# Kernel tuning notes

Measured on AMD Instinct MI355X. Metric: run time of the kernel, lower is better.

Reference implementation:

```python
import jax, jax.numpy as jnp
import numpy as np
from jax import lax

B, S, I = 256, 16, 64
D = 128
N_ITEMS = 100000
K = 3
PAD_ID = 0
BOS_ID = N_ITEMS
DILATIONS = (1, 2, 4)


def setup_inputs() -> dict:
    key = jax.random.key(0)
    ks = jax.random.split(key, 16)
    item_id = jax.random.randint(ks[0], (B, S, I), 0, N_ITEMS, dtype=jnp.int32)
    eval_from = jax.random.randint(ks[1], (B,), 0, S, dtype=jnp.int32)
    u_type = jax.random.randint(ks[2], (B,), 0, 4, dtype=jnp.int32)
    emb = jax.random.normal(ks[3], (N_ITEMS + 1, D), jnp.float32) * 0.05
    emb = emb.at[PAD_ID].set(0.0)  # padding_idx=0
    kaiming = (2.0 / (D * K)) ** 0.5
    conv_w0 = jax.random.normal(ks[4], (D, D, K), jnp.float32) * kaiming
    conv_w1 = jax.random.normal(ks[5], (D, D, K), jnp.float32) * kaiming
    conv_w2 = jax.random.normal(ks[6], (D, D, K), jnp.float32) * kaiming
    conv_b0 = jnp.zeros((D,), jnp.float32)
    conv_b1 = jnp.zeros((D,), jnp.float32)
    conv_b2 = jnp.zeros((D,), jnp.float32)
    gru_wih = jax.random.normal(ks[7], (3 * D, D), jnp.float32) * 0.05
    gru_whh = jax.random.normal(ks[8], (3 * D, D), jnp.float32) * 0.05
    gru_bih = jax.random.normal(ks[9], (3 * D,), jnp.float32) * 0.05
    gru_bhh = jax.random.normal(ks[10], (3 * D,), jnp.float32) * 0.05
    fus_w = jax.random.normal(ks[11], (D, 2 * D), jnp.float32) * 0.05
    fus_b = jnp.zeros((D,), jnp.float32)
    return {"item_id": item_id, "eval_from": eval_from, "u_type": u_type,
            "emb": emb,
            "conv_w0": conv_w0, "conv_b0": conv_b0,
            "conv_w1": conv_w1, "conv_b1": conv_b1,
            "conv_w2": conv_w2, "conv_b2": conv_b2,
            "gru_wih": gru_wih, "gru_whh": gru_whh,
            "gru_bih": gru_bih, "gru_bhh": gru_bhh,
            "fus_w": fus_w, "fus_b": fus_b}


def reference(item_id, eval_from, u_type, emb,
              conv_w0, conv_b0, conv_w1, conv_b1, conv_w2, conv_b2,
              gru_wih, gru_whh, gru_bih, gru_bhh, fus_w, fus_b):
    item_id = jnp.maximum(item_id, 0)  # clamp_min(0)
    Bc, Sc, Ic = item_id.shape
    convs = ((conv_w0, conv_b0, DILATIONS[0]),
             (conv_w1, conv_b1, DILATIONS[1]),
             (conv_w2, conv_b2, DILATIONS[2]))

    def tcn(x):  # x: [B, T, D] -> [B, T, D]
        h = jnp.transpose(x, (0, 2, 1))  # NCH
        for w, b, dil in convs:
            pad = (K - 1) * dil
            out = lax.conv_general_dilated(
                h, w, window_strides=(1,), padding=[(pad, 0)],
                rhs_dilation=(dil,),
                dimension_numbers=('NCH', 'OIH', 'NCH')) + b[None, :, None]
            h = jax.nn.relu(out + h)
        return jnp.transpose(h, (0, 2, 1))

    def gru_step(h, x):  # h,x: [B, D]
        gi = x @ gru_wih.T + gru_bih
        gh = h @ gru_whh.T + gru_bhh
        ir, iz, inn = jnp.split(gi, 3, axis=-1)
        hr, hz, hn = jnp.split(gh, 3, axis=-1)
        r = jax.nn.sigmoid(ir + hr)
        z = jax.nn.sigmoid(iz + hz)
        n = jnp.tanh(inn + r * hn)
        return (1.0 - z) * n + z * h

    pos = jnp.arange(Ic + 1)
    bos = jnp.full((Bc, 1), BOS_ID, dtype=item_id.dtype)

    def step(h, seq_s):  # seq_s: [B, I]
        lengths = (seq_s != PAD_ID).sum(-1)          # [B]
        max_len = lengths.max()                       # batch-level session max
        seq = jnp.concatenate([bos, seq_s], axis=1)   # [B, I+1], BOS prepended
        valid = pos[None, :] <= max_len               # positions torch keeps
        seq = jnp.where(valid, seq, PAD_ID)
        mask = seq != PAD_ID
        e = emb[seq]                                  # [B, I+1, D] (PAD row is 0)
        tc = tcn(e)
        fin = jnp.concatenate([tc, jnp.broadcast_to(h[:, None, :], tc.shape)], -1)
        reps = fin @ fus_w.T + fus_b                  # [B, I+1, D]
        reps = reps * valid[..., None]                # torch zero-pads beyond max_len
        # drop mask at last valid token (per-sample python loop in torch)
        mask = mask & ~((pos[None, :] == lengths[:, None]) & (lengths > 0)[:, None])
        mf = mask.astype(e.dtype)
        mean_emb = (e * mf[..., None]).sum(1) / jnp.maximum(mf.sum(1), 1.0)[:, None]
        h2 = gru_step(h, mean_emb)
        return h2, (reps, mask)

    h0 = jnp.zeros((Bc, D), jnp.float32)
    _, (reps, masks) = lax.scan(step, h0, jnp.transpose(item_id, (1, 0, 2)))
    reps = jnp.transpose(reps, (1, 0, 2, 3))          # [B, S, I+1, D]
    masks = jnp.transpose(masks, (1, 0, 2))           # [B, S, I+1]
    allow = jnp.arange(Sc)[None, :] >= eval_from[:, None]
    loss_masks = masks & allow[:, :, None]
    return reps, loss_masks, u_type
```

## Files before the change

kernel.cpp:

```cpp
#include <hip/hip_runtime.h>

#define BB 256
#define SS 16
#define II 64
#define DD 128
#define TT 65
#define BOS_ID 100000
#define RB 88
#define XBYTES (RB*256)

#define OFF_LEN  0
#define OFF_ML   16384
#define OFF_ME   32768
#define OFF_HB   (32768 + 2097152)
#define OFF_WB   (OFF_HB + 2097152)
#define OFF_FT   (OFF_WB + 294912)
#define OFF_WIHP (OFF_FT + 32768)
#define OFF_WGRU (OFF_WIHP + 98304)
#define OFF_GI   (OFF_WGRU + 131072)

#define OUT_MASK  (BB*SS*TT*DD)
#define OUT_UTYPE (OUT_MASK + BB*SS*TT)

typedef __attribute__((ext_vector_type(8))) short short8;
typedef __attribute__((ext_vector_type(4))) float f32x4;

__device__ __forceinline__ unsigned short f2bf(float f) {
    unsigned int u = __builtin_bit_cast(unsigned int, f);
    return (unsigned short)((u + 0x7fffu + ((u >> 16) & 1u)) >> 16);
}
__device__ __forceinline__ float bf2f(unsigned short h) {
    unsigned int u = ((unsigned int)h) << 16;
    return __builtin_bit_cast(float, u);
}
__device__ __forceinline__ void gld16(const void* g, void* l) {
    __builtin_amdgcn_global_load_lds(
        (const __attribute__((address_space(1))) void*)g,
        (__attribute__((address_space(3))) void*)l, 16, 0, 0);
}

__global__ __launch_bounds__(256) void prep_kernel(
    const float* __restrict__ w0, const float* __restrict__ w1,
    const float* __restrict__ w2, const float* __restrict__ fus_w,
    const float* __restrict__ wih, const float* __restrict__ whh,
    unsigned short* __restrict__ wB, unsigned short* __restrict__ fT,
    unsigned int* __restrict__ wihP, unsigned int* __restrict__ wgruP)
{
    int idx = blockIdx.x * 256 + threadIdx.x;
    if (idx < 147456) {
        int L  = idx / 49152;
        int r  = idx % 49152;
        int k  = r >> 14;
        int co = (r >> 7) & 127;
        int ci = r & 127;
        const float* w = (L == 0) ? w0 : ((L == 1) ? w1 : w2);
        float v = w[(co * 128 + ci) * 3 + k];
        wB[((L * 3 + k) * 128 + co) * 128 + (ci ^ ((co & 7) << 3))] = f2bf(v);
    } else if (idx < 163840) {
        int f  = idx - 147456;
        int j  = f >> 7;
        int ci = f & 127;
        fT[(j << 7) | (ci ^ ((j & 7) << 3))] = f2bf(fus_w[j * 256 + ci]);
    } else if (idx < 163840 + 24576) {
        int f  = idx - 163840;
        int dd = f / 384;
        int r  = f % 384;
        unsigned int lo = f2bf(wih[r * 128 + 2 * dd]);
        unsigned int hi = f2bf(wih[r * 128 + 2 * dd + 1]);
        wihP[f] = (hi << 16) | lo;
    } else if (idx < 163840 + 24576 + 32768) {
        int f  = idx - 163840 - 24576;
        int dd = f >> 9;
        int r  = f & 511;
        float v0, v1;
        if (r < 384) { v0 = whh[r * 128 + 2 * dd]; v1 = whh[r * 128 + 2 * dd + 1]; }
        else { const float* fw = fus_w + (r - 384) * 256 + 128;
               v0 = fw[2 * dd]; v1 = fw[2 * dd + 1]; }
        wgruP[f] = ((unsigned int)f2bf(v1) << 16) | (unsigned int)f2bf(v0);
    }
}

__global__ __launch_bounds__(256) void len_kernel(
    const int* __restrict__ item_id, const int* __restrict__ u_type,
    int* __restrict__ lengths, int* __restrict__ maxlen,
    float* __restrict__ u_out)
{
    int s = blockIdx.x;
    int b = threadIdx.x;
    const int* row = item_id + (b * SS + s) * II;
    int cnt = 0;
    for (int i = 0; i < II; ++i) cnt += (row[i] > 0);
    lengths[b * SS + s] = cnt;
    __shared__ int red[256];
    red[b] = cnt;
    __syncthreads();
    for (int off = 128; off > 0; off >>= 1) {
        if (b < off) red[b] = max(red[b], red[b + off]);
        __syncthreads();
    }
    if (b == 0) maxlen[s] = red[0];
    if (s == 0) u_out[b] = (float)u_type[b];
}

__global__ __launch_bounds__(128) void mean_kernel(
    const int* __restrict__ item_id, const int* __restrict__ eval_from,
    const float* __restrict__ emb,
    const int* __restrict__ lengths, const int* __restrict__ maxlen,
    float* __restrict__ mean_emb, float* __restrict__ mask_out)
{
    int bid = blockIdx.x;
    int b = bid >> 4, s = bid & 15;
    int tid = threadIdx.x;
    __shared__ int seqs[TT];
    __shared__ int msk[TT];
    int ml  = maxlen[s];
    int len = lengths[bid];
    int ef  = eval_from[b];
    if (tid < TT) {
        int v;
        if (tid == 0) v = BOS_ID;
        else { int it = item_id[bid * II + tid - 1]; v = it > 0 ? it : 0; }
        if (tid > ml) v = 0;
        int m = (v != 0) && !(tid == len && len > 0);
        seqs[tid] = v;
        msk[tid]  = m;
        mask_out[bid * TT + tid] = (m && (s >= ef)) ? 1.0f : 0.0f;
    }
    __syncthreads();
    int cnt = 0;
    for (int p = 0; p < TT; ++p) cnt += msk[p];
    float acc = 0.0f;
    int d = tid;
    for (int p = 0; p < TT; ++p) {
        if (msk[p]) acc += emb[seqs[p] * DD + d];
    }
    mean_emb[bid * DD + d] = acc / (float)max(cnt, 1);
}

__global__ __launch_bounds__(384, 1) void gi_kernel(
    const float* __restrict__ me_all, const unsigned int* __restrict__ wihP,
    const float* __restrict__ bih, float* __restrict__ gi_all)
{
    __shared__ __align__(16) unsigned int wl[64 * 384];
    __shared__ __align__(16) float me[DD];
    int t   = threadIdx.x;
    int blk = blockIdx.x;
    {
        const unsigned char* g = (const unsigned char*)wihP + t * 16;
        unsigned char* l = (unsigned char*)wl + t * 16;
#pragma unroll
        for (int i = 0; i < 16; ++i) gld16(g + i * 6144, l + i * 6144);
    }
    float bi = bih[t];
    asm volatile("s_waitcnt vmcnt(0)" ::: "memory");
    __syncthreads();
    for (int q = 0; q < 16; ++q) {
        int bs = blk * 16 + q;
        if (t < DD) me[t] = me_all[bs * DD + t];
        __syncthreads();
        float acc = bi;
#pragma unroll
        for (int dd = 0; dd < 64; ++dd) {
            unsigned int u = wl[dd * 384 + t];
            float f0 = __builtin_bit_cast(float, u << 16);
            float f1 = __builtin_bit_cast(float, u & 0xffff0000u);
            acc += f0 * me[2 * dd] + f1 * me[2 * dd + 1];
        }
        gi_all[bs * 384 + t] = acc;
        __syncthreads();
    }
}

__global__ __launch_bounds__(512, 1) void gru_kernel(
    const unsigned int* __restrict__ wgruP, const float* __restrict__ bhh,
    const float* __restrict__ fus_b, const float* __restrict__ gi_all,
    float* __restrict__ hB)
{
    __shared__ __align__(16) unsigned int wl[64 * 512];
    __shared__ float h[DD];
    __shared__ float g_z[DD], g_inn[DD], g_hn[DD];
    int t = threadIdx.x;
    int b = blockIdx.x;
    int j = t & 127;
    int grp = t >> 7;
    {
        const unsigned char* g = (const unsigned char*)wgruP + t * 16;
        unsigned char* l = (unsigned char*)wl + t * 16;
#pragma unroll
        for (int i = 0; i < 16; ++i) gld16(g + i * 8192, l + i * 8192);
    }
    float bias = (t < 384) ? bhh[t] : fus_b[j];
    if (t < DD) h[t] = 0.0f;
    asm volatile("s_waitcnt vmcnt(0)" ::: "memory");
    __syncthreads();
    for (int s = 0; s < SS; ++s) {
        float gi = (grp < 3) ? gi_all[(b * SS + s) * 384 + t] : 0.0f;
        float acc = bias;
#pragma unroll
        for (int dd = 0; dd < 64; ++dd) {
            unsigned int u = wl[dd * 512 + t];
            float f0 = __builtin_bit_cast(float, u << 16);
            float f1 = __builtin_bit_cast(float, u & 0xffff0000u);
            acc += f0 * h[2 * dd] + f1 * h[2 * dd + 1];
        }
        if (grp == 3) {
            hB[(s * BB + b) * DD + j] = acc;
        } else if (grp == 1) { g_z[j] = gi + acc; }
        else if (grp == 2)   { g_inn[j] = gi; g_hn[j] = acc; }
        __syncthreads();
        if (grp == 0) {
            float r = 1.0f / (1.0f + expf(-(gi + acc)));
            float z = 1.0f / (1.0f + expf(-g_z[j]));
            float n = tanhf(g_inn[j] + r * g_hn[j]);
            h[j] = (1.0f - z) * n + z * h[j];
        }
        __syncthreads();
    }
}

__global__ __launch_bounds__(256) void tcn_kernel(
    const int* __restrict__ item_id, const float* __restrict__ emb,
    const int* __restrict__ maxlen,
    const unsigned short* __restrict__ wB,
    const float* __restrict__ cb0, const float* __restrict__ cb1,
    const float* __restrict__ cb2,
    const unsigned short* __restrict__ fT, const float* __restrict__ hB,
    float* __restrict__ reps)
{
    __shared__ __align__(16) unsigned char xbufA[XBYTES];
    __shared__ __align__(16) unsigned char xbufB[XBYTES];
    __shared__ __align__(16) unsigned char wl[32768];
    __shared__ int seqs[TT];

    int tid  = threadIdx.x;
    int bid  = blockIdx.x;
    int b    = bid >> 4, s = bid & 15;
    int lane = tid & 63, wv = tid >> 6;
    int ml   = maxlen[s];

    if (tid < TT) {
        int v;
        if (tid == 0) v = BOS_ID;
        else { int it = item_id[bid * II + tid - 1]; v = it > 0 ? it : 0; }
        if (tid > ml) v = 0;
        seqs[tid] = v;
    }
    if (tid < 128) { *(unsigned int*)(xbufA + tid * 16) = 0u;
                     *(unsigned int*)(xbufA + tid * 16 + 4) = 0u;
                     *(unsigned int*)(xbufA + tid * 16 + 8) = 0u;
                     *(unsigned int*)(xbufA + tid * 16 + 12) = 0u; }
    else { int t = tid - 128;
           *(unsigned int*)(xbufB + t * 16) = 0u;
           *(unsigned int*)(xbufB + t * 16 + 4) = 0u;
           *(unsigned int*)(xbufB + t * 16 + 8) = 0u;
           *(unsigned int*)(xbufB + t * 16 + 12) = 0u; }
    __syncthreads();

    for (int p = wv; p < TT; p += 4) {
        const float* er = emb + (long)seqs[p] * DD + lane * 2;
        float f0 = er[0], f1 = er[1];
        int row = 8 + p;
        unsigned int pk = ((unsigned int)f2bf(f1) << 16) | (unsigned int)f2bf(f0);
        *(unsigned int*)(xbufA + row * 256 + ((lane * 4) ^ ((row & 7) << 4))) = pk;
    }

    unsigned char* xsrc = xbufA;
    unsigned char* ydst = xbufB;
    int co0  = wv * 32;
    int colb = (lane >> 4) * 16;

    f32x4 acc[5][2];

    for (int L = 0; L < 3; ++L) {
        int dil = 1 << L;
        const float* cb = (L == 0) ? cb0 : ((L == 1) ? cb1 : cb2);
#pragma unroll
        for (int mt = 0; mt < 5; ++mt)
#pragma unroll
            for (int nt = 0; nt < 2; ++nt)
#pragma unroll
                for (int r = 0; r < 4; ++r) acc[mt][nt][r] = 0.0f;

        for (int k = 0; k < 3; ++k) {
            __syncthreads();
            {
                const unsigned char* g =
                    (const unsigned char*)wB + (size_t)(L * 3 + k) * 32768 +
                    (wv * 64 + lane) * 16;
#pragma unroll
                for (int i = 0; i < 8; ++i)
                    gld16(g + i * 4096, wl + wv * 1024 + i * 4096);
            }
            asm volatile("s_waitcnt vmcnt(0)" ::: "memory");
            __syncthreads();

            int off = (2 - k) * dil;
#pragma unroll
            for (int cib = 0; cib < 4; ++cib) {
                int cbyte = cib * 64 + colb;
                short8 bfr[2];
#pragma unroll
                for (int nt = 0; nt < 2; ++nt) {
                    int rowB = co0 + nt * 16 + (lane & 15);
                    bfr[nt] = *(const short8*)(wl + rowB * 256 +
                                               (cbyte ^ ((rowB & 7) << 4)));
                }
#pragma unroll
                for (int mt = 0; mt < 5; ++mt) {
                    int rowA = 8 + mt * 16 + (lane & 15) - off;
                    short8 af = *(const short8*)(xsrc + rowA * 256 +
                                                 (cbyte ^ ((rowA & 7) << 4)));
                    acc[mt][0] = __builtin_amdgcn_mfma_f32_16x16x32_bf16(
                        af, bfr[0], acc[mt][0], 0, 0, 0);
                    acc[mt][1] = __builtin_amdgcn_mfma_f32_16x16x32_bf16(
                        af, bfr[1], acc[mt][1], 0, 0, 0);
                }
            }
        }
        float bias0 = cb[co0 + (lane & 15)];
        float bias1 = cb[co0 + 16 + (lane & 15)];
#pragma unroll
        for (int mt = 0; mt < 5; ++mt)
#pragma unroll
            for (int nt = 0; nt < 2; ++nt) {
                int co = co0 + nt * 16 + (lane & 15);
                float bia = nt ? bias1 : bias0;
#pragma unroll
                for (int r = 0; r < 4; ++r) {
                    int p = mt * 16 + (lane >> 4) * 4 + r;
                    if (p < TT) {
                        int row = 8 + p;
                        int xb2 = row * 256 + ((co * 2) ^ ((row & 7) << 4));
                        float v = acc[mt][nt][r] + bia +
                                  bf2f(*(const unsigned short*)(xsrc + xb2));
                        *(unsigned short*)(ydst + xb2) = f2bf(v > 0.f ? v : 0.f);
                    }
                }
            }
        unsigned char* t = xsrc; xsrc = ydst; ydst = t;
    }

    __syncthreads();
    {
        const unsigned char* g = (const unsigned char*)fT + (wv * 64 + lane) * 16;
#pragma unroll
        for (int i = 0; i < 8; ++i)
            gld16(g + i * 4096, wl + wv * 1024 + i * 4096);
    }
    asm volatile("s_waitcnt vmcnt(0)" ::: "memory");
    __syncthreads();

#pragma unroll
    for (int mt = 0; mt < 5; ++mt)
#pragma unroll
        for (int nt = 0; nt < 2; ++nt)
#pragma unroll
            for (int r = 0; r < 4; ++r) acc[mt][nt][r] = 0.0f;

#pragma unroll
    for (int cib = 0; cib < 4; ++cib) {
        int cbyte = cib * 64 + colb;
        short8 bfr[2];
#pragma unroll
        for (int nt = 0; nt < 2; ++nt) {
            int rowB = co0 + nt * 16 + (lane & 15);
            bfr[nt] = *(const short8*)(wl + rowB * 256 + (cbyte ^ ((rowB & 7) << 4)));
        }
#pragma unroll
        for (int mt = 0; mt < 5; ++mt) {
            int rowA = 8 + mt * 16 + (lane & 15);
            short8 af = *(const short8*)(xsrc + rowA * 256 +
                                         (cbyte ^ ((rowA & 7) << 4)));
            acc[mt][0] = __builtin_amdgcn_mfma_f32_16x16x32_bf16(
                af, bfr[0], acc[mt][0], 0, 0, 0);
            acc[mt][1] = __builtin_amdgcn_mfma_f32_16x16x32_bf16(
                af, bfr[1], acc[mt][1], 0, 0, 0);
        }
    }

    float hb0 = hB[(s * BB + b) * DD + co0 + (lane & 15)];
    float hb1 = hB[(s * BB + b) * DD + co0 + 16 + (lane & 15)];
    long obase = (long)bid * (TT * DD);
#pragma unroll
    for (int mt = 0; mt < 5; ++mt)
#pragma unroll
        for (int nt = 0; nt < 2; ++nt) {
            int j = co0 + nt * 16 + (lane & 15);
            float hb = nt ? hb1 : hb0;
#pragma unroll
            for (int r = 0; r < 4; ++r) {
                int p = mt * 16 + (lane >> 4) * 4 + r;
                if (p < TT) {
                    float v = (p <= ml) ? (acc[mt][nt][r] + hb) : 0.0f;
                    reps[obase + p * DD + j] = v;
                }
            }
        }
}

extern "C" void kernel_launch(void* const* d_in, const int* in_sizes, int n_in,
                              void* d_out, int out_size, void* d_ws, size_t ws_size,
                              hipStream_t stream) {
    const int*   item_id   = (const int*)  d_in[0];
    const int*   eval_from = (const int*)  d_in[1];
    const int*   u_type    = (const int*)  d_in[2];
    const float* emb       = (const float*)d_in[3];
    const float* conv_w0   = (const float*)d_in[4];
    const float* conv_b0   = (const float*)d_in[5];
    const float* conv_w1   = (const float*)d_in[6];
    const float* conv_b1   = (const float*)d_in[7];
    const float* conv_w2   = (const float*)d_in[8];
    const float* conv_b2   = (const float*)d_in[9];
    const float* gru_wih   = (const float*)d_in[10];
    const float* gru_whh   = (const float*)d_in[11];
    const float* gru_bih   = (const float*)d_in[12];
    const float* gru_bhh   = (const float*)d_in[13];
    const float* fus_w     = (const float*)d_in[14];
    const float* fus_b     = (const float*)d_in[15];

    char* ws = (char*)d_ws;
    int*            lengths  = (int*)           (ws + OFF_LEN);
    int*            maxlen   = (int*)           (ws + OFF_ML);
    float*          mean_emb = (float*)         (ws + OFF_ME);
    float*          hB       = (float*)         (ws + OFF_HB);
    unsigned short* wB       = (unsigned short*)(ws + OFF_WB);
    unsigned short* fT       = (unsigned short*)(ws + OFF_FT);
    unsigned int*   wihP     = (unsigned int*)  (ws + OFF_WIHP);
    unsigned int*   wgruP    = (unsigned int*)  (ws + OFF_WGRU);
    float*          gi_all   = (float*)         (ws + OFF_GI);

    float* out  = (float*)d_out;
    float* reps = out;
    float* mout = out + OUT_MASK;
    float* uout = out + OUT_UTYPE;

    prep_kernel<<<864, 256, 0, stream>>>(conv_w0, conv_w1, conv_w2, fus_w,
                                         gru_wih, gru_whh, wB, fT, wihP, wgruP);
    len_kernel<<<SS, 256, 0, stream>>>(item_id, u_type, lengths, maxlen, uout);
    mean_kernel<<<BB * SS, 128, 0, stream>>>(item_id, eval_from, emb, lengths, maxlen,
                                             mean_emb, mout);
    gi_kernel<<<BB, 384, 0, stream>>>(mean_emb, wihP, gru_bih, gi_all);
    gru_kernel<<<BB, 512, 0, stream>>>(wgruP, gru_bhh, fus_b, gi_all, hB);
    tcn_kernel<<<BB * SS, 256, 0, stream>>>(item_id, emb, maxlen, wB,
                                            conv_b0, conv_b1, conv_b2, fT, hB, reps);
}
```

Measured before the change: 292.6 us.

## Restructure TCN kernel: two tiles per block, per-wave double-buffered weight streaming

Each block of the TCN kernel now handles two (b,s) tiles, with a pair of waves per tile and each wave owning 64 output channels. Weights are pre-packed into per-wave 8 KB chunks covering conv layers and the fusion matrix, and streamed through a per-wave double-buffered LDS ring with async global-to-LDS loads. This removes most block-wide barriers and overlaps weight loads with MFMA work. Activations are updated in place in padded rows instead of an XOR swizzle with ping-pong buffers, and launch bounds request 2 blocks per CU. In exchange, each thread holds more accumulator registers and the LDS padding scheme must avoid bank conflicts.

```diff
diff --git a/kernel.cpp b/kernel.cpp
--- a/kernel.cpp
+++ b/kernel.cpp
@@ -6,16 +6,16 @@
 #define DD 128
 #define TT 65
 #define BOS_ID 100000
-#define RB 88
-#define XBYTES (RB*256)
+#define XROW 304
+#define XROWS 73
+#define XT (XROWS*XROW)
 
 #define OFF_LEN  0
 #define OFF_ML   16384
 #define OFF_ME   32768
 #define OFF_HB   (32768 + 2097152)
-#define OFF_WB   (OFF_HB + 2097152)
-#define OFF_FT   (OFF_WB + 294912)
-#define OFF_WIHP (OFF_FT + 32768)
+#define OFF_WB2  (OFF_HB + 2097152)
+#define OFF_WIHP (OFF_WB2 + 327680)
 #define OFF_WGRU (OFF_WIHP + 98304)
 #define OFF_GI   (OFF_WGRU + 131072)
 
@@ -43,24 +43,32 @@
     const float* __restrict__ w0, const float* __restrict__ w1,
     const float* __restrict__ w2, const float* __restrict__ fus_w,
     const float* __restrict__ wih, const float* __restrict__ whh,
-    unsigned short* __restrict__ wB, unsigned short* __restrict__ fT,
+    unsigned short* __restrict__ wB2,
     unsigned int* __restrict__ wihP, unsigned int* __restrict__ wgruP)
 {
     int idx = blockIdx.x * 256 + threadIdx.x;
-    if (idx < 147456) {
-        int L  = idx / 49152;
-        int r  = idx % 49152;
-        int k  = r >> 14;
-        int co = (r >> 7) & 127;
-        int ci = r & 127;
-        const float* w = (L == 0) ? w0 : ((L == 1) ? w1 : w2);
-        float v = w[(co * 128 + ci) * 3 + k];
-        wB[((L * 3 + k) * 128 + co) * 128 + (ci ^ ((co & 7) << 3))] = f2bf(v);
-    } else if (idx < 163840) {
-        int f  = idx - 147456;
-        int j  = f >> 7;
-        int ci = f & 127;
-        fT[(j << 7) | (ci ^ ((j & 7) << 3))] = f2bf(fus_w[j * 256 + ci]);
+    if (idx < 163840) {
+        int cid2  = idx >> 11;
+        int inner = idx & 2047;
+        int g = inner >> 9;
+        int c = (inner >> 3) & 63;
+        int e = inner & 7;
+        int nh   = cid2 & 1;
+        int rest = cid2 >> 1;
+        int cq   = rest & 3;
+        int m    = rest >> 2;
+        int ci = cq * 32 + g * 8 + e;
+        float v;
+        if (m < 9) {
+            int L = m / 3, k = m % 3;
+            int co = nh * 64 + c;
+            const float* w = (L == 0) ? w0 : ((L == 1) ? w1 : w2);
+            v = w[(co * 128 + ci) * 3 + k];
+        } else {
+            int j = nh * 64 + c;
+            v = fus_w[j * 256 + ci];
+        }
+        wB2[idx] = f2bf(v);
     } else if (idx < 163840 + 24576) {
         int f  = idx - 163840;
         int dd = f / 384;
@@ -218,181 +226,142 @@
     }
 }
 
-__global__ __launch_bounds__(256) void tcn_kernel(
+__global__ __launch_bounds__(256, 2) void tcn_kernel(
     const int* __restrict__ item_id, const float* __restrict__ emb,
     const int* __restrict__ maxlen,
-    const unsigned short* __restrict__ wB,
+    const unsigned short* __restrict__ wB2,
     const float* __restrict__ cb0, const float* __restrict__ cb1,
     const float* __restrict__ cb2,
-    const unsigned short* __restrict__ fT, const float* __restrict__ hB,
-    float* __restrict__ reps)
-{
-    __shared__ __align__(16) unsigned char xbufA[XBYTES];
-    __shared__ __align__(16) unsigned char xbufB[XBYTES];
-    __shared__ __align__(16) unsigned char wl[32768];
-    __shared__ int seqs[TT];
-
-    int tid  = threadIdx.x;
-    int bid  = blockIdx.x;
-    int b    = bid >> 4, s = bid & 15;
-    int lane = tid & 63, wv = tid >> 6;
-    int ml   = maxlen[s];
-
-    if (tid < TT) {
+    const float* __restrict__ hB, float* __restrict__ reps)
+{
+    __shared__ __align__(16) unsigned char lds_x[2][XT];
+    __shared__ __align__(16) unsigned char ring[4][2][4096];
+    __shared__ int seqs2[2][TT];
+
+    const int tid = threadIdx.x, bid = blockIdx.x;
+    const int lane = tid & 63, wv = tid >> 6;
+    const int l15 = lane & 15, q4 = lane >> 4;
+    const int t = wv >> 1, nh = wv & 1;
+    const int tile = bid * 2 + t;
+    const int b = tile >> 4, s = tile & 15;
+    const int ml = maxlen[s];
+
+    const unsigned char* wsrc = (const unsigned char*)wB2 + nh * 4096 + lane * 16;
+    unsigned char* xb = lds_x[t];
+
+    {
+#pragma unroll
+        for (int i = 0; i < 4; ++i) gld16(wsrc + i * 1024, &ring[wv][0][i * 1024]);
+#pragma unroll
+        for (int i = 0; i < 4; ++i) gld16(wsrc + 8192 + i * 1024, &ring[wv][1][i * 1024]);
+    }
+
+    if (tid < 2 * TT) {
+        int tt = tid / TT, p = tid - tt * TT;
+        int tl = bid * 2 + tt;
         int v;
-        if (tid == 0) v = BOS_ID;
-        else { int it = item_id[bid * II + tid - 1]; v = it > 0 ? it : 0; }
-        if (tid > ml) v = 0;
-        seqs[tid] = v;
-    }
-    if (tid < 128) { *(unsigned int*)(xbufA + tid * 16) = 0u;
-                     *(unsigned int*)(xbufA + tid * 16 + 4) = 0u;
-                     *(unsigned int*)(xbufA + tid * 16 + 8) = 0u;
-                     *(unsigned int*)(xbufA + tid * 16 + 12) = 0u; }
-    else { int t = tid - 128;
-           *(unsigned int*)(xbufB + t * 16) = 0u;
-           *(unsigned int*)(xbufB + t * 16 + 4) = 0u;
-           *(unsigned int*)(xbufB + t * 16 + 8) = 0u;
-           *(unsigned int*)(xbufB + t * 16 + 12) = 0u; }
-    __syncthreads();
-
-    for (int p = wv; p < TT; p += 4) {
-        const float* er = emb + (long)seqs[p] * DD + lane * 2;
+        if (p == 0) v = BOS_ID;
+        else { int it = item_id[tl * II + p - 1]; v = it > 0 ? it : 0; }
+        if (p > maxlen[tl & 15]) v = 0;
+        seqs2[tt][p] = v;
+    }
+    for (int i = tid; i < 608; i += 256) {
+        *(unsigned int*)(lds_x[0] + i * 4) = 0u;
+        *(unsigned int*)(lds_x[1] + i * 4) = 0u;
+    }
+    __syncthreads();
+
+    for (int p = nh; p < TT; p += 2) {
+        const float* er = emb + (long)seqs2[t][p] * DD + lane * 2;
         float f0 = er[0], f1 = er[1];
-        int row = 8 + p;
         unsigned int pk = ((unsigned int)f2bf(f1) << 16) | (unsigned int)f2bf(f0);
-        *(unsigned int*)(xbufA + row * 256 + ((lane * 4) ^ ((row & 7) << 4))) = pk;
-    }
-
-    unsigned char* xsrc = xbufA;
-    unsigned char* ydst = xbufB;
-    int co0  = wv * 32;
-    int colb = (lane >> 4) * 16;
-
-    f32x4 acc[5][2];
-
-    for (int L = 0; L < 3; ++L) {
-        int dil = 1 << L;
-        const float* cb = (L == 0) ? cb0 : ((L == 1) ? cb1 : cb2);
+        *(unsigned int*)(xb + (8 + p) * XROW + lane * 4) = pk;
+    }
+
+    float bias[3][4], hb[4];
+#pragma unroll
+    for (int nt = 0; nt < 4; ++nt) {
+        int co = nh * 64 + nt * 16 + l15;
+        bias[0][nt] = cb0[co]; bias[1][nt] = cb1[co]; bias[2][nt] = cb2[co];
+        hb[nt] = hB[(s * BB + b) * DD + co];
+    }
+    __syncthreads();
+
+    f32x4 acc[5][4];
+
+#pragma unroll 1
+    for (int cid = 0; cid < 40; ++cid) {
+        int L = 0, cq, off, kq = 0;
+        if (cid < 36) { L = cid / 12; kq = cid - L * 12; int k = kq >> 2; cq = kq & 3; off = (2 - k) << L; }
+        else { cq = cid - 36; off = 0; }
+        if (cid == 36 || (cid < 36 && kq == 0)) {
+#pragma unroll
+            for (int mt = 0; mt < 5; ++mt)
+#pragma unroll
+                for (int nt = 0; nt < 4; ++nt)
+#pragma unroll
+                    for (int r = 0; r < 4; ++r) acc[mt][nt][r] = 0.0f;
+        }
+        if (cid < 39) asm volatile("s_waitcnt vmcnt(4)" ::: "memory");
+        else          asm volatile("s_waitcnt vmcnt(0)" ::: "memory");
+
+        const unsigned char* sb = &ring[wv][cid & 1][0];
+        short8 bfr[4], af[5];
+#pragma unroll
+        for (int nt = 0; nt < 4; ++nt)
+            bfr[nt] = *(const short8*)(sb + q4 * 1024 + (nt * 16 + l15) * 16);
+#pragma unroll
+        for (int mt = 0; mt < 5; ++mt) {
+            int rowA = 8 + mt * 16 + l15 - off;
+            af[mt] = *(const short8*)(xb + rowA * XROW + cq * 64 + q4 * 16);
+        }
+        asm volatile("s_waitcnt lgkmcnt(0)" ::: "memory");
+        __builtin_amdgcn_sched_barrier(0);
+        if (cid <= 37) {
+            const unsigned char* src = wsrc + (size_t)(cid + 2) * 8192;
+#pragma unroll
+            for (int i = 0; i < 4; ++i) gld16(src + i * 1024, &ring[wv][cid & 1][i * 1024]);
+        }
 #pragma unroll
         for (int mt = 0; mt < 5; ++mt)
 #pragma unroll
-            for (int nt = 0; nt < 2; ++nt)
-#pragma unroll
-                for (int r = 0; r < 4; ++r) acc[mt][nt][r] = 0.0f;
-
-        for (int k = 0; k < 3; ++k) {
+            for (int nt = 0; nt < 4; ++nt)
+                acc[mt][nt] = __builtin_amdgcn_mfma_f32_16x16x32_bf16(
+                    af[mt], bfr[nt], acc[mt][nt], 0, 0, 0);
+
+        if (cid < 36 && kq == 11) {
             __syncthreads();
-            {
-                const unsigned char* g =
-                    (const unsigned char*)wB + (size_t)(L * 3 + k) * 32768 +
-                    (wv * 64 + lane) * 16;
-#pragma unroll
-                for (int i = 0; i < 8; ++i)
-                    gld16(g + i * 4096, wl + wv * 1024 + i * 4096);
-            }
-            asm volatile("s_waitcnt vmcnt(0)" ::: "memory");
-            __syncthreads();
-
-            int off = (2 - k) * dil;
-#pragma unroll
-            for (int cib = 0; cib < 4; ++cib) {
-                int cbyte = cib * 64 + colb;
-                short8 bfr[2];
-#pragma unroll
-                for (int nt = 0; nt < 2; ++nt) {
-                    int rowB = co0 + nt * 16 + (lane & 15);
-                    bfr[nt] = *(const short8*)(wl + rowB * 256 +
-                                               (cbyte ^ ((rowB & 7) << 4)));
-                }
-#pragma unroll
-                for (int mt = 0; mt < 5; ++mt) {
-                    int rowA = 8 + mt * 16 + (lane & 15) - off;
-                    short8 af = *(const short8*)(xsrc + rowA * 256 +
-                                                 (cbyte ^ ((rowA & 7) << 4)));
-                    acc[mt][0] = __builtin_amdgcn_mfma_f32_16x16x32_bf16(
-                        af, bfr[0], acc[mt][0], 0, 0, 0);
-                    acc[mt][1] = __builtin_amdgcn_mfma_f32_16x16x32_bf16(
-                        af, bfr[1], acc[mt][1], 0, 0, 0);
-                }
-            }
-        }
-        float bias0 = cb[co0 + (lane & 15)];
-        float bias1 = cb[co0 + 16 + (lane & 15)];
-#pragma unroll
-        for (int mt = 0; mt < 5; ++mt)
-#pragma unroll
-            for (int nt = 0; nt < 2; ++nt) {
-                int co = co0 + nt * 16 + (lane & 15);
-                float bia = nt ? bias1 : bias0;
-#pragma unroll
-                for (int r = 0; r < 4; ++r) {
-                    int p = mt * 16 + (lane >> 4) * 4 + r;
-                    if (p < TT) {
-                        int row = 8 + p;
-                        int xb2 = row * 256 + ((co * 2) ^ ((row & 7) << 4));
-                        float v = acc[mt][nt][r] + bia +
-                                  bf2f(*(const unsigned short*)(xsrc + xb2));
-                        *(unsigned short*)(ydst + xb2) = f2bf(v > 0.f ? v : 0.f);
+#pragma unroll
+            for (int mt = 0; mt < 5; ++mt)
+#pragma unroll
+                for (int nt = 0; nt < 4; ++nt) {
+#pragma unroll
+                    for (int r = 0; r < 4; ++r) {
+                        int p = mt * 16 + q4 * 4 + r;
+                        if (p < TT) {
+                            int addr = (8 + p) * XROW + nh * 128 + (nt * 16 + l15) * 2;
+                            float v = acc[mt][nt][r] + bias[L][nt] +
+                                      bf2f(*(const unsigned short*)(xb + addr));
+                            *(unsigned short*)(xb + addr) = f2bf(v > 0.f ? v : 0.f);
+                        }
                     }
                 }
-            }
-        unsigned char* t = xsrc; xsrc = ydst; ydst = t;
-    }
-
-    __syncthreads();
-    {
-        const unsigned char* g = (const unsigned char*)fT + (wv * 64 + lane) * 16;
-#pragma unroll
-        for (int i = 0; i < 8; ++i)
-            gld16(g + i * 4096, wl + wv * 1024 + i * 4096);
-    }
-    asm volatile("s_waitcnt vmcnt(0)" ::: "memory");
-    __syncthreads();
-
+            __syncthreads();
+        }
+    }
+
+    long ob = (long)tile * (TT * DD);
 #pragma unroll
     for (int mt = 0; mt < 5; ++mt)
 #pragma unroll
-        for (int nt = 0; nt < 2; ++nt)
-#pragma unroll
-            for (int r = 0; r < 4; ++r) acc[mt][nt][r] = 0.0f;
-
-#pragma unroll
-    for (int cib = 0; cib < 4; ++cib) {
-        int cbyte = cib * 64 + colb;
-        short8 bfr[2];
-#pragma unroll
-        for (int nt = 0; nt < 2; ++nt) {
-            int rowB = co0 + nt * 16 + (lane & 15);
-            bfr[nt] = *(const short8*)(wl + rowB * 256 + (cbyte ^ ((rowB & 7) << 4)));
-        }
-#pragma unroll
-        for (int mt = 0; mt < 5; ++mt) {
-            int rowA = 8 + mt * 16 + (lane & 15);
-            short8 af = *(const short8*)(xsrc + rowA * 256 +
-                                         (cbyte ^ ((rowA & 7) << 4)));
-            acc[mt][0] = __builtin_amdgcn_mfma_f32_16x16x32_bf16(
-                af, bfr[0], acc[mt][0], 0, 0, 0);
-            acc[mt][1] = __builtin_amdgcn_mfma_f32_16x16x32_bf16(
-                af, bfr[1], acc[mt][1], 0, 0, 0);
-        }
-    }
-
-    float hb0 = hB[(s * BB + b) * DD + co0 + (lane & 15)];
-    float hb1 = hB[(s * BB + b) * DD + co0 + 16 + (lane & 15)];
-    long obase = (long)bid * (TT * DD);
-#pragma unroll
-    for (int mt = 0; mt < 5; ++mt)
-#pragma unroll
-        for (int nt = 0; nt < 2; ++nt) {
-            int j = co0 + nt * 16 + (lane & 15);
-            float hb = nt ? hb1 : hb0;
+        for (int nt = 0; nt < 4; ++nt) {
+            int co = nh * 64 + nt * 16 + l15;
 #pragma unroll
             for (int r = 0; r < 4; ++r) {
-                int p = mt * 16 + (lane >> 4) * 4 + r;
+                int p = mt * 16 + q4 * 4 + r;
                 if (p < TT) {
-                    float v = (p <= ml) ? (acc[mt][nt][r] + hb) : 0.0f;
-                    reps[obase + p * DD + j] = v;
+                    float v = (p <= ml) ? (acc[mt][nt][r] + hb[nt]) : 0.0f;
+                    reps[ob + p * DD + co] = v;
                 }
             }
         }
@@ -423,8 +392,7 @@
     int*            maxlen   = (int*)           (ws + OFF_ML);
     float*          mean_emb = (float*)         (ws + OFF_ME);
     float*          hB       = (float*)         (ws + OFF_HB);
-    unsigned short* wB       = (unsigned short*)(ws + OFF_WB);
-    unsigned short* fT       = (unsigned short*)(ws + OFF_FT);
+    unsigned short* wB2      = (unsigned short*)(ws + OFF_WB2);
     unsigned int*   wihP     = (unsigned int*)  (ws + OFF_WIHP);
     unsigned int*   wgruP    = (unsigned int*)  (ws + OFF_WGRU);
     float*          gi_all   = (float*)         (ws + OFF_GI);
@@ -435,12 +403,12 @@
     float* uout = out + OUT_UTYPE;
 
     prep_kernel<<<864, 256, 0, stream>>>(conv_w0, conv_w1, conv_w2, fus_w,
-                                         gru_wih, gru_whh, wB, fT, wihP, wgruP);
+                                         gru_wih, gru_whh, wB2, wihP, wgruP);
     len_kernel<<<SS, 256, 0, stream>>>(item_id, u_type, lengths, maxlen, uout);
     mean_kernel<<<BB * SS, 128, 0, stream>>>(item_id, eval_from, emb, lengths, maxlen,
                                              mean_emb, mout);
     gi_kernel<<<BB, 384, 0, stream>>>(mean_emb, wihP, gru_bih, gi_all);
     gru_kernel<<<BB, 512, 0, stream>>>(wgruP, gru_bhh, fus_b, gi_all, hB);
-    tcn_kernel<<<BB * SS, 256, 0, stream>>>(item_id, emb, maxlen, wB,
-                                            conv_b0, conv_b1, conv_b2, fT, hB, reps);
-}
+    tcn_kernel<<<BB * SS / 2, 256, 0, stream>>>(item_id, emb, maxlen, wB2,
+                                                conv_b0, conv_b1, conv_b2, hB, reps);
+}
```

New measurement: 269.4 us. -7.9%, faster.
